# Kernel tuning notes

Measured on AMD Instinct MI355X. Metric: run time of the kernel, lower is better.

## Reference

```python
import jax, jax.numpy as jnp
import numpy as np

B = 2048
NU, NF, NA = 20000, 100000, 20000  # users, feeds, authors
D = 150   # SVD embed dim for FM features
DK = 64   # tag/keyword/d2v embed dim


def setup_inputs() -> dict:
    key = jax.random.key(0)
    ks = jax.random.split(key, 24)
    r = lambda k, shape: (jax.random.normal(k, shape, dtype=jnp.float32) * 0.05)
    # ids: user, feed, author columns with their own vocab ranges
    u = jax.random.randint(ks[0], (B,), 0, NU)
    f = jax.random.randint(ks[1], (B,), 0, NF)
    a = jax.random.randint(ks[2], (B,), 0, NA)
    inputs = jnp.stack([u, f, a], axis=1).astype(jnp.int32)  # [B,3]
    first_order_shifts = jnp.array([0, NU, NU + NF], dtype=jnp.int32)
    return {
        'inputs': inputs,
        'first_order_shifts': first_order_shifts,
        'W_user_feed': r(ks[3], (NU, D)),
        'W_feed_user': r(ks[4], (NF, D)),
        'W_user_author': r(ks[5], (NU, D)),
        'W_author_user': r(ks[6], (NA, D)),
        'W_feed_emb': r(ks[7], (NF, D)),          # trainable=False in original
        'W_user_tag': r(ks[8], (NU, DK)),
        'W_user_key1': r(ks[9], (NU, DK)),
        'W_user_key2': r(ks[10], (NU, DK)),
        'W_feed_tag': r(ks[11], (NF, DK)),
        'W_feed_key1': r(ks[12], (NF, DK)),
        'W_feed_key2': r(ks[13], (NF, DK)),
        'W_uf_d2v': r(ks[14], (NU, DK)),
        'W_fu_d2v': r(ks[15], (NF, DK)),
        'W_ua_d2v': r(ks[16], (NU, DK)),
        'W_au_d2v': r(ks[17], (NA, DK)),
        'W256': r(ks[18], (2 * D * D, 256)),       # 45000 -> 256
        'b256': jnp.zeros((256,), jnp.float32),
        'W128': r(ks[19], (2 * DK * DK, 128)),     # 8192 -> 128
        'b128': jnp.zeros((128,), jnp.float32),
    }


def reference(inputs, first_order_shifts, W_user_feed, W_feed_user,
              W_user_author, W_author_user, W_feed_emb, W_user_tag,
              W_user_key1, W_user_key2, W_feed_tag, W_feed_key1, W_feed_key2,
              W_uf_d2v, W_fu_d2v, W_ua_d2v, W_au_d2v, W256, b256, W128, b128):
    inputs = inputs.reshape(-1, 3)
    u, f, a = inputs[:, 0], inputs[:, 1], inputs[:, 2]
    one_hot_inputs = inputs + first_order_shifts[None, :]

    user_feed_embed = W_user_feed[u]      # [B,150]
    user_author_embed = W_user_author[u]
    author_user_embed = W_author_user[a]
    feed_emb_embed = W_feed_emb[f]
    feed_user_embed = W_feed_user[f]
    user_tag_embed = W_user_tag[u]        # [B,64]
    user_key1_embed = W_user_key1[u]
    user_key2_embed = W_user_key2[u]
    feed_tag_embed = W_feed_tag[f]
    feed_key1_embed = W_feed_key1[f]
    feed_key2_embed = W_feed_key2[f]
    user_feed_d2vem = W_uf_d2v[u]
    user_author_d2vem = W_ua_d2v[u]
    feed_user_d2vem = W_fu_d2v[f]
    author_user_d2vem = W_au_d2v[a]

    # d2v outer products -> [B,64,64] each; concat axis=1 -> [B,128,64]
    user_w_feed = jnp.einsum('bi,bj->bij', user_feed_d2vem, feed_user_d2vem)
    user_w_auth = jnp.einsum('bi,bj->bij', user_author_d2vem, author_user_d2vem)
    user_w_user = jnp.concatenate([user_w_feed, user_w_auth], axis=1)
    user_w_user = user_w_user.reshape(-1, 2 * DK * DK)
    user_w_user = jax.nn.relu(user_w_user @ W128 + b128)  # Dropout inactive (inference)

    # SVD outer products -> [B,150,150] each; concat axis=1 -> [B,300,150]
    user_x_feed = jnp.einsum('bi,bj->bij', user_feed_embed, feed_user_embed)
    user_x_auth = jnp.einsum('bi,bj->bij', user_author_embed, author_user_embed)
    user_x_user = jnp.concatenate([user_x_feed, user_x_auth], axis=1)
    user_x_user = user_x_user.reshape(-1, 2 * D * D)
    user_x_user = jax.nn.relu(user_x_user @ W256 + b256)

    # tf.concat([list], axis=1) stacks the inner list -> [4,B,150], then reshape (-1,4,150)
    embeds_fm = jnp.stack([user_feed_embed, user_author_embed,
                           feed_user_embed, author_user_embed], axis=0)
    fm_embed_inputs = embeds_fm.reshape(-1, 4, D)

    expert_inputs = jnp.concatenate([
        user_feed_embed, user_author_embed, user_tag_embed, user_key1_embed,
        user_key2_embed, user_feed_d2vem, user_author_d2vem, feed_user_embed,
        feed_tag_embed, feed_key1_embed, feed_emb_embed, feed_key2_embed,
        feed_user_d2vem, author_user_embed, author_user_d2vem,
        user_x_user, user_w_user], axis=-1)  # [B,1710]
    return expert_inputs, one_hot_inputs, fm_embed_inputs
```

## Files before the change

### kernel.cpp

```cpp
#include <hip/hip_runtime.h>
#include <hip/hip_bf16.h>
#include <stdint.h>

#define BB   2048
#define DD   150
#define DKK  64

static constexpr int EXPERT_W  = 1774;
static constexpr int X_OFF     = 1390;
static constexpr int W_OFF     = 1646;
static constexpr int EXPERT_SZ = BB * EXPERT_W;
static constexpr int OH_BASE   = EXPERT_SZ;
static constexpr int FM_BASE   = OH_BASE + BB * 3;

static constexpr size_t WTX_OFF = 0;
static constexpr size_t WTW_OFF = 24576000;
static constexpr size_t WSX_OFF = 26673152;
static constexpr size_t WSW_OFF = 60227584;
static constexpr size_t WS_NEED = 77004800;

typedef __attribute__((ext_vector_type(8))) short bf16x8;
typedef __attribute__((ext_vector_type(4))) float f32x4;

union APack { int d[4]; bf16x8 v; };

__device__ __forceinline__ int cvtpk_bf16(float a, float b) {
  int r; asm("v_cvt_pk_bf16_f32 %0, %1, %2" : "=v"(r) : "v"(a), "v"(b)); return r;
}
__device__ __forceinline__ f32x4 mfma16(bf16x8 a, bf16x8 b, f32x4 c) {
  return __builtin_amdgcn_mfma_f32_16x16x32_bf16(a, b, c, 0, 0, 0);
}
__device__ __forceinline__ void gload16(const void* g, void* l) {
  __builtin_amdgcn_global_load_lds(
      (__attribute__((address_space(1))) void*)(g),
      (__attribute__((address_space(3))) void*)(l), 16, 0, 0);
}

__global__ __launch_bounds__(256) void gather_kernel(
    const int* __restrict__ inputs, const int* __restrict__ shifts,
    const float* __restrict__ Wuf, const float* __restrict__ Wfu,
    const float* __restrict__ Wua, const float* __restrict__ Wau,
    const float* __restrict__ Wfe,
    const float* __restrict__ Wut, const float* __restrict__ Wuk1, const float* __restrict__ Wuk2,
    const float* __restrict__ Wft, const float* __restrict__ Wfk1, const float* __restrict__ Wfk2,
    const float* __restrict__ Wufd, const float* __restrict__ Wfud,
    const float* __restrict__ Wuad, const float* __restrict__ Waud,
    float* __restrict__ out)
{
    const int b = blockIdx.x;
    const int u = inputs[b*3 + 0];
    const int f = inputs[b*3 + 1];
    const int a = inputs[b*3 + 2];
    float* row = out + b * EXPERT_W;
    float* fm  = out + FM_BASE;
    const int t = threadIdx.x;

    for (int c = t; c < DD; c += 256) {
        float ufe = Wuf[u*DD + c];
        float uae = Wua[u*DD + c];
        float fue = Wfu[f*DD + c];
        float fee = Wfe[f*DD + c];
        float aue = Wau[a*DD + c];
        row[0    + c] = ufe;
        row[150  + c] = uae;
        row[620  + c] = fue;
        row[898  + c] = fee;
        row[1176 + c] = aue;
        fm[0*BB*DD + b*DD + c] = ufe;
        fm[1*BB*DD + b*DD + c] = uae;
        fm[2*BB*DD + b*DD + c] = fue;
        fm[3*BB*DD + b*DD + c] = aue;
    }
    for (int c = t; c < DKK; c += 256) {
        row[300  + c] = Wut [u*DKK + c];
        row[364  + c] = Wuk1[u*DKK + c];
        row[428  + c] = Wuk2[u*DKK + c];
        row[492  + c] = Wufd[u*DKK + c];
        row[556  + c] = Wuad[u*DKK + c];
        row[770  + c] = Wft [f*DKK + c];
        row[834  + c] = Wfk1[f*DKK + c];
        row[1048 + c] = Wfk2[f*DKK + c];
        row[1112 + c] = Wfud[f*DKK + c];
        row[1326 + c] = Waud[a*DKK + c];
    }
    if (t < 3) {
        out[OH_BASE + b*3 + t] = (float)(inputs[b*3 + t] + shifts[t]);
    }
}

__global__ __launch_bounds__(256) void tile_pack_x(
    const float* __restrict__ W, __hip_bfloat16* __restrict__ Wt)
{
  const int T  = blockIdx.x;
  const int jj = T / 300;
  const int i  = T - jj*300;
  const int t  = threadIdx.x;
  float v[32];
  const float* src = W + ((size_t)i*150 + jj*32)*256 + t;
  #pragma unroll
  for (int jl = 0; jl < 32; ++jl) {
    int j = jj*32 + jl;
    v[jl] = (j < 150) ? src[(size_t)jl*256] : 0.f;
  }
  const int blk = t >> 4, nloc = t & 15;
  char* dst = (char*)Wt + (size_t)T*16384 + (size_t)(blk*512 + nloc*8)*2;
  #pragma unroll
  for (int ksub = 0; ksub < 4; ++ksub) {
    int pk0 = cvtpk_bf16(v[ksub*8+0], v[ksub*8+1]);
    int pk1 = cvtpk_bf16(v[ksub*8+2], v[ksub*8+3]);
    int pk2 = cvtpk_bf16(v[ksub*8+4], v[ksub*8+5]);
    int pk3 = cvtpk_bf16(v[ksub*8+6], v[ksub*8+7]);
    *(int4*)(dst + (size_t)ksub*256) = make_int4(pk0, pk1, pk2, pk3);
  }
}

__global__ __launch_bounds__(128) void tile_pack_w(
    const float* __restrict__ W, __hip_bfloat16* __restrict__ Wt)
{
  const int T  = blockIdx.x;
  const int jj = T >> 7;
  const int i  = T & 127;
  const int t  = threadIdx.x;
  float v[32];
  const float* src = W + ((size_t)i*64 + jj*32)*128 + t;
  #pragma unroll
  for (int jl = 0; jl < 32; ++jl) v[jl] = src[(size_t)jl*128];
  const int blk = t >> 4, nloc = t & 15;
  char* dst = (char*)Wt + (size_t)T*8192 + (size_t)(blk*512 + nloc*8)*2;
  #pragma unroll
  for (int ksub = 0; ksub < 4; ++ksub) {
    int pk0 = cvtpk_bf16(v[ksub*8+0], v[ksub*8+1]);
    int pk1 = cvtpk_bf16(v[ksub*8+2], v[ksub*8+3]);
    int pk2 = cvtpk_bf16(v[ksub*8+4], v[ksub*8+5]);
    int pk3 = cvtpk_bf16(v[ksub*8+6], v[ksub*8+7]);
    *(int4*)(dst + (size_t)ksub*256) = make_int4(pk0, pk1, pk2, pk3);
  }
}

__global__ __launch_bounds__(512, 4) void xuser_mfma(
    const int* __restrict__ inputs,
    const float* __restrict__ Wuf, const float* __restrict__ Wua,
    const float* __restrict__ Wfu, const float* __restrict__ Wau,
    const __hip_bfloat16* __restrict__ WtXt, float* __restrict__ wsX)
{
  __shared__ float xlds[128*20];
  __shared__ __align__(16) __hip_bfloat16 blds[2][8192];

  const int bid = blockIdx.x;
  const int h  = bid & 1;
  const int s  = (bid >> 1) & 15;
  const int mb = bid >> 5;
  const int b0 = mb * 128;
  const bool upper = s >= 8;
  const int sl  = upper ? s - 8 : s;
  const int i0l = sl * 19;
  const int cnt = (150 - i0l) < 19 ? (150 - i0l) : 19;
  const int ig0 = i0l + (upper ? 150 : 0);
  const int tid = threadIdx.x;

  const float* X = upper ? Wua : Wuf;
  const float* Y = upper ? Wau : Wfu;
  const int yoff = upper ? 2 : 1;

  for (int k = tid; k < 128*20; k += 512) {
    int r = k / 20, ii = k - r*20;
    float v = 0.f;
    if (ii < cnt) v = X[(size_t)inputs[(b0+r)*3]*150 + i0l + ii];
    xlds[k] = v;
  }

  const int lane = tid & 63;
  const int w  = tid >> 6;
  const int mg = w >> 1;
  const int ng = w & 1;
  const int lr = lane & 15;
  const int g  = lane >> 4;

  int yid[2];
  #pragma unroll
  for (int mf = 0; mf < 2; ++mf)
    yid[mf] = inputs[(size_t)(b0 + mg*32 + mf*16 + lr)*3 + yoff];

  const char* wtb = (const char*)WtXt + (size_t)h*8192;
  const unsigned wdst = (unsigned)(tid & ~63) * 16;

  auto stageT = [&](int bufi, int T) {
    const char* sp = wtb + (size_t)T*16384 + (size_t)tid*16;
    char* dp = (char*)&blds[bufi][0] + wdst;
    gload16(sp,         dp);
    gload16(sp + 16384, dp + 8192);
  };

  f32x4 acc[2][4];
  #pragma unroll
  for (int i = 0; i < 2; ++i)
    #pragma unroll
    for (int j = 0; j < 4; ++j) acc[i][j] = (f32x4){0.f,0.f,0.f,0.f};

  const int PJ = (cnt + 1) >> 1;
  const int P  = 5 * PJ;

  stageT(0, ig0);
  stageT(1, ig0 + 2);

  int jjc = 0, iic = 0;
  int jjs = 0, iis = 4;
  int yjj = -1;
  float yreg[2][8];

  for (int p = 0; p < P; ++p) {
    if (jjc != yjj) {
      yjj = jjc;
      const int jb = jjc*32 + g*8;
      #pragma unroll
      for (int mf = 0; mf < 2; ++mf) {
        const float* yp = Y + (size_t)yid[mf]*150;
        if (jb + 8 <= 150) {
          #pragma unroll
          for (int hh = 0; hh < 4; ++hh) {
            float2 vv = *(const float2*)(yp + jb + 2*hh);
            yreg[mf][2*hh]   = vv.x;
            yreg[mf][2*hh+1] = vv.y;
          }
        } else {
          #pragma unroll
          for (int e = 0; e < 8; ++e)
            yreg[mf][e] = (jb + e < 150) ? yp[jb + e] : 0.f;
        }
      }
    }
    if (p + 1 < P) asm volatile("s_waitcnt vmcnt(2)" ::: "memory");
    else           asm volatile("s_waitcnt vmcnt(0)" ::: "memory");
    __builtin_amdgcn_s_barrier();
    __builtin_amdgcn_sched_barrier(0);

    const int buf = p & 1;
    const int rem = cnt - iic;
    #pragma unroll
    for (int sc = 0; sc < 2; ++sc) {
      if (sc == 1 && rem < 2) break;
      const __hip_bfloat16* bb = &blds[buf][sc*4096];
      bf16x8 bv[4];
      #pragma unroll
      for (int nf = 0; nf < 4; ++nf)
        bv[nf] = *(const bf16x8*)(bb + (ng*4 + nf)*512 + g*128 + lr*8);
      APack a[2];
      #pragma unroll
      for (int mf = 0; mf < 2; ++mf) {
        float xv = xlds[(mg*32 + mf*16 + lr)*20 + iic + sc];
        #pragma unroll
        for (int e = 0; e < 4; ++e)
          a[mf].d[e] = cvtpk_bf16(xv*yreg[mf][2*e], xv*yreg[mf][2*e+1]);
      }
      #pragma unroll
      for (int mf = 0; mf < 2; ++mf)
        #pragma unroll
        for (int nf = 0; nf < 4; ++nf)
          acc[mf][nf] = mfma16(a[mf].v, bv[nf], acc[mf][nf]);
    }

    __builtin_amdgcn_s_barrier();
    if (p + 2 < P) stageT(buf, jjs*300 + ig0 + iis);

    iic += 2; if (iic >= cnt) { iic = 0; ++jjc; }
    iis += 2; if (iis >= cnt) { iis = 0; ++jjs; }
  }

  float* wp = wsX + ((size_t)s*2048 + b0)*256;
  #pragma unroll
  for (int mf = 0; mf < 2; ++mf) {
    #pragma unroll
    for (int nf = 0; nf < 4; ++nf) {
      int rb  = mg*32 + mf*16 + g*4;
      int col = h*128 + ng*64 + nf*16 + lr;
      f32x4 v = acc[mf][nf];
      #pragma unroll
      for (int e = 0; e < 4; ++e) wp[(size_t)(rb+e)*256 + col] = v[e];
    }
  }
}

__global__ __launch_bounds__(512, 4) void wuser_mfma(
    const int* __restrict__ inputs,
    const float* __restrict__ Wufd, const float* __restrict__ Wuad,
    const float* __restrict__ Wfud, const float* __restrict__ Waud,
    const __hip_bfloat16* __restrict__ WtWt, float* __restrict__ wsW)
{
  __shared__ float xlds[128*8];
  __shared__ __align__(16) __hip_bfloat16 blds[2][8192];

  const int mb = blockIdx.x >> 4;
  const int s  = blockIdx.x & 15;
  const int b0 = mb * 128;
  const bool upper = s >= 8;
  const int i0l = (s & 7) * 8;
  const int ig0 = i0l + (upper ? 64 : 0);
  const int tid = threadIdx.x;

  const float* X = upper ? Wuad : Wufd;
  const float* Y = upper ? Waud : Wfud;
  const int yoff = upper ? 2 : 1;

  for (int k = tid; k < 128*8; k += 512) {
    int r = k >> 3, ii = k & 7;
    xlds[k] = X[(size_t)inputs[(size_t)(b0+r)*3]*64 + i0l + ii];
  }

  const int lane = tid & 63;
  const int w  = tid >> 6;
  const int mg = w >> 1;
  const int ng = w & 1;
  const int lr = lane & 15;
  const int g  = lane >> 4;

  int yid[2];
  #pragma unroll
  for (int mf = 0; mf < 2; ++mf)
    yid[mf] = inputs[(size_t)(b0 + mg*32 + mf*16 + lr)*3 + yoff];

  const char* wtb = (const char*)WtWt;
  const unsigned wdst = (unsigned)(tid & ~63) * 16;

  auto stageT = [&](int bufi, int T) {
    const char* sp = wtb + (size_t)T*8192 + (size_t)tid*16;
    char* dp = (char*)&blds[bufi][0] + wdst;
    gload16(sp,        dp);
    gload16(sp + 8192, dp + 8192);
  };

  f32x4 acc[2][4];
  #pragma unroll
  for (int i = 0; i < 2; ++i)
    #pragma unroll
    for (int j = 0; j < 4; ++j) acc[i][j] = (f32x4){0.f,0.f,0.f,0.f};

  stageT(0, ig0);
  stageT(1, ig0 + 2);

  int jjc = 0, iic = 0;
  int jjs = 0, iis = 4;
  int yjj = -1;
  float yreg[2][8];

  for (int p = 0; p < 8; ++p) {
    if (jjc != yjj) {
      yjj = jjc;
      const int jb = jjc*32 + g*8;
      #pragma unroll
      for (int mf = 0; mf < 2; ++mf) {
        const float* yp = Y + (size_t)yid[mf]*64 + jb;
        #pragma unroll
        for (int hh = 0; hh < 2; ++hh) {
          float4 v = *(const float4*)(yp + hh*4);
          yreg[mf][hh*4]   = v.x;
          yreg[mf][hh*4+1] = v.y;
          yreg[mf][hh*4+2] = v.z;
          yreg[mf][hh*4+3] = v.w;
        }
      }
    }
    if (p + 1 < 8) asm volatile("s_waitcnt vmcnt(2)" ::: "memory");
    else           asm volatile("s_waitcnt vmcnt(0)" ::: "memory");
    __builtin_amdgcn_s_barrier();
    __builtin_amdgcn_sched_barrier(0);

    const int buf = p & 1;
    #pragma unroll
    for (int sc = 0; sc < 2; ++sc) {
      const __hip_bfloat16* bb = &blds[buf][sc*4096];
      bf16x8 bv[4];
      #pragma unroll
      for (int nf = 0; nf < 4; ++nf)
        bv[nf] = *(const bf16x8*)(bb + (ng*4 + nf)*512 + g*128 + lr*8);
      APack a[2];
      #pragma unroll
      for (int mf = 0; mf < 2; ++mf) {
        float xv = xlds[(mg*32 + mf*16 + lr)*8 + iic + sc];
        #pragma unroll
        for (int e = 0; e < 4; ++e)
          a[mf].d[e] = cvtpk_bf16(xv*yreg[mf][2*e], xv*yreg[mf][2*e+1]);
      }
      #pragma unroll
      for (int mf = 0; mf < 2; ++mf)
        #pragma unroll
        for (int nf = 0; nf < 4; ++nf)
          acc[mf][nf] = mfma16(a[mf].v, bv[nf], acc[mf][nf]);
    }

    __builtin_amdgcn_s_barrier();
    if (p + 2 < 8) stageT(buf, jjs*128 + ig0 + iis);

    iic += 2; if (iic >= 8) { iic = 0; ++jjc; }
    iis += 2; if (iis >= 8) { iis = 0; ++jjs; }
  }

  float* wp = wsW + ((size_t)s*2048 + b0)*128;
  #pragma unroll
  for (int mf = 0; mf < 2; ++mf) {
    #pragma unroll
    for (int nf = 0; nf < 4; ++nf) {
      int rb  = mg*32 + mf*16 + g*4;
      int col = ng*64 + nf*16 + lr;
      f32x4 v = acc[mf][nf];
      #pragma unroll
      for (int e = 0; e < 4; ++e) wp[(size_t)(rb+e)*128 + col] = v[e];
    }
  }
}

__global__ __launch_bounds__(256) void epilogue_kernel(
    const float* __restrict__ wsX, const float* __restrict__ wsW,
    const float* __restrict__ b256, const float* __restrict__ b128,
    float* __restrict__ out)
{
  int idx = blockIdx.x*256 + threadIdx.x;
  if (idx >= BB*384) return;
  int b = idx / 384, c = idx - b*384;
  if (c < 256) {
    float acc = b256[c];
    #pragma unroll
    for (int k = 0; k < 16; ++k) acc += wsX[((size_t)k*BB + b)*256 + c];
    out[(size_t)b*EXPERT_W + X_OFF + c] = acc > 0.f ? acc : 0.f;
  } else {
    int cc = c - 256;
    float acc = b128[cc];
    #pragma unroll
    for (int k = 0; k < 16; ++k) acc += wsW[((size_t)k*BB + b)*128 + cc];
    out[(size_t)b*EXPERT_W + W_OFF + cc] = acc > 0.f ? acc : 0.f;
  }
}

static constexpr int NPAIR_X = 300 * 150;
static constexpr int CHX     = 128;

__global__ __launch_bounds__(256) void xuser_kernel(
    const int* __restrict__ inputs,
    const float* __restrict__ Wuf, const float* __restrict__ Wua,
    const float* __restrict__ Wfu, const float* __restrict__ Wau,
    const float* __restrict__ W256, const float* __restrict__ b256,
    float* __restrict__ out)
{
    __shared__ float xs[16][308];
    __shared__ float ys[16][308];
    __shared__ float xy[CHX][16];
    const int half = blockIdx.x & 1;
    const int bg   = blockIdx.x >> 1;
    const int b0   = bg * 16;
    const int t    = threadIdx.x;
    const int bl   = t & 15;
    const int kg   = t >> 4;
    const int kbase = half * 128 + kg * 8;
    for (int idx = t; idx < 16 * DD; idx += 256) {
        int bb = idx / DD;
        int c  = idx - bb * DD;
        int u = inputs[(b0+bb)*3 + 0];
        int f = inputs[(b0+bb)*3 + 1];
        int a = inputs[(b0+bb)*3 + 2];
        xs[bb][c]       = Wuf[u*DD + c];
        xs[bb][150 + c] = Wua[u*DD + c];
        ys[bb][c]       = Wfu[f*DD + c];
        ys[bb][150 + c] = Wau[a*DD + c];
    }
    float acc[8] = {0,0,0,0,0,0,0,0};
    for (int base = 0; base < NPAIR_X; base += CHX) {
        __syncthreads();
        #pragma unroll
        for (int r = 0; r < (CHX*16)/256; ++r) {
            int idx = t + r * 256;
            int pl  = idx >> 4;
            int bb  = idx & 15;
            int p   = base + pl;
            if (p < NPAIR_X) {
                int i = p / 150;
                int j = p - i * 150;
                xy[pl][bb] = xs[bb][i] * ys[bb][(i >= 150 ? 150 : 0) + j];
            }
        }
        __syncthreads();
        const int lim = min(CHX, NPAIR_X - base);
        const float* wp = W256 + base * 256 + kbase;
        for (int pl = 0; pl < lim; ++pl) {
            float sv = xy[pl][bl];
            const float4* w4 = (const float4*)(wp + pl * 256);
            float4 w0 = w4[0], w1 = w4[1];
            acc[0] = fmaf(sv, w0.x, acc[0]); acc[1] = fmaf(sv, w0.y, acc[1]);
            acc[2] = fmaf(sv, w0.z, acc[2]); acc[3] = fmaf(sv, w0.w, acc[3]);
            acc[4] = fmaf(sv, w1.x, acc[4]); acc[5] = fmaf(sv, w1.y, acc[5]);
            acc[6] = fmaf(sv, w1.z, acc[6]); acc[7] = fmaf(sv, w1.w, acc[7]);
        }
    }
    const int rowbase = (b0 + bl) * EXPERT_W + X_OFF;
    #pragma unroll
    for (int m = 0; m < 8; ++m) {
        float v = acc[m] + b256[kbase + m];
        out[rowbase + kbase + m] = (v > 0.f ? v : 0.f);
    }
}

static constexpr int NPAIR_W = 128 * 64;
static constexpr int CHW     = 256;

__global__ __launch_bounds__(256) void wuser_kernel(
    const int* __restrict__ inputs,
    const float* __restrict__ Wufd, const float* __restrict__ Wuad,
    const float* __restrict__ Wfud, const float* __restrict__ Waud,
    const float* __restrict__ W128, const float* __restrict__ b128,
    float* __restrict__ out)
{
    __shared__ float xs[8][132];
    __shared__ float ys[8][132];
    __shared__ float xy[CHW][8];
    const int bg = blockIdx.x;
    const int b0 = bg * 8;
    const int t  = threadIdx.x;
    const int bl = t & 7;
    const int kg = t >> 3;
    const int kbase = kg * 4;
    for (int idx = t; idx < 8 * DKK; idx += 256) {
        int bb = idx >> 6;
        int c  = idx & 63;
        int u = inputs[(b0+bb)*3 + 0];
        int f = inputs[(b0+bb)*3 + 1];
        int a = inputs[(b0+bb)*3 + 2];
        xs[bb][c]      = Wufd[u*DKK + c];
        xs[bb][64 + c] = Wuad[u*DKK + c];
        ys[bb][c]      = Wfud[f*DKK + c];
        ys[bb][64 + c] = Waud[a*DKK + c];
    }
    float acc[4] = {0,0,0,0};
    for (int base = 0; base < NPAIR_W; base += CHW) {
        __syncthreads();
        #pragma unroll
        for (int r = 0; r < (CHW*8)/256; ++r) {
            int idx = t + r * 256;
            int pl  = idx >> 3;
            int bb  = idx & 7;
            int p   = base + pl;
            int i = p >> 6;
            int j = p & 63;
            xy[pl][bb] = xs[bb][i] * ys[bb][(i >= 64 ? 64 : 0) + j];
        }
        __syncthreads();
        const float* wp = W128 + base * 128 + kbase;
        for (int pl = 0; pl < CHW; ++pl) {
            float sv = xy[pl][bl];
            float4 wv = *(const float4*)(wp + pl * 128);
            acc[0] = fmaf(sv, wv.x, acc[0]); acc[1] = fmaf(sv, wv.y, acc[1]);
            acc[2] = fmaf(sv, wv.z, acc[2]); acc[3] = fmaf(sv, wv.w, acc[3]);
        }
    }
    const int rowbase = (b0 + bl) * EXPERT_W + W_OFF;
    #pragma unroll
    for (int m = 0; m < 4; ++m) {
        float v = acc[m] + b128[kbase + m];
        out[rowbase + kbase + m] = (v > 0.f ? v : 0.f);
    }
}

extern "C" void kernel_launch(void* const* d_in, const int* in_sizes, int n_in,
                              void* d_out, int out_size, void* d_ws, size_t ws_size,
                              hipStream_t stream)
{
    const int*   inputs = (const int*)  d_in[0];
    const int*   shifts = (const int*)  d_in[1];
    const float* Wuf    = (const float*)d_in[2];
    const float* Wfu    = (const float*)d_in[3];
    const float* Wua    = (const float*)d_in[4];
    const float* Wau    = (const float*)d_in[5];
    const float* Wfe    = (const float*)d_in[6];
    const float* Wut    = (const float*)d_in[7];
    const float* Wuk1   = (const float*)d_in[8];
    const float* Wuk2   = (const float*)d_in[9];
    const float* Wft    = (const float*)d_in[10];
    const float* Wfk1   = (const float*)d_in[11];
    const float* Wfk2   = (const float*)d_in[12];
    const float* Wufd   = (const float*)d_in[13];
    const float* Wfud   = (const float*)d_in[14];
    const float* Wuad   = (const float*)d_in[15];
    const float* Waud   = (const float*)d_in[16];
    const float* W256   = (const float*)d_in[17];
    const float* b256   = (const float*)d_in[18];
    const float* W128   = (const float*)d_in[19];
    const float* b128   = (const float*)d_in[20];

    float* out = (float*)d_out;

    gather_kernel<<<BB, 256, 0, stream>>>(inputs, shifts,
        Wuf, Wfu, Wua, Wau, Wfe, Wut, Wuk1, Wuk2, Wft, Wfk1, Wfk2,
        Wufd, Wfud, Wuad, Waud, out);

    if (ws_size >= WS_NEED) {
        char* ws = (char*)d_ws;
        __hip_bfloat16* WtX = (__hip_bfloat16*)(ws + WTX_OFF);
        __hip_bfloat16* WtW = (__hip_bfloat16*)(ws + WTW_OFF);
        float* wsX = (float*)(ws + WSX_OFF);
        float* wsW = (float*)(ws + WSW_OFF);

        tile_pack_x<<<1500, 256, 0, stream>>>(W256, WtX);
        tile_pack_w<<<256, 128, 0, stream>>>(W128, WtW);

        xuser_mfma<<<512, 512, 0, stream>>>(inputs, Wuf, Wua, Wfu, Wau, WtX, wsX);
        wuser_mfma<<<256, 512, 0, stream>>>(inputs, Wufd, Wuad, Wfud, Waud, WtW, wsW);

        epilogue_kernel<<<(BB*384 + 255)/256, 256, 0, stream>>>(wsX, wsW, b256, b128, out);
    } else {
        xuser_kernel<<<256, 256, 0, stream>>>(inputs, Wuf, Wua, Wfu, Wau, W256, b256, out);
        wuser_kernel<<<256, 256, 0, stream>>>(inputs, Wufd, Wuad, Wfud, Waud, W128, b128, out);
    }
}
```

Baseline: 105.7 us.

## Switch X-path GEMM to 32x32x16 MFMA with 2x4 wave tiling

Replaces the 16x16x32 bf16 MFMA tiles in the user-x-user projection kernel with 32x32x16 MFMAs. Waves are remapped from a 4x2 to a 2x4 grid, and the outer-product A-operand construction and output scatter are reworked for the larger tile. This reduces the number of MFMA issues and B-fragment LDS reads per step. The double-buffer prefetch is also changed from a two-deep vmcnt-based pipeline to a one-ahead stage with __syncthreads, which may expose more global-load latency.

Measured after the change: 121.6 us. +15.0%, slower.

```diff
diff --git a/kernel.cpp b/kernel.cpp
--- a/kernel.cpp
+++ b/kernel.cpp
@@ -19,8 +19,9 @@
 static constexpr size_t WSW_OFF = 60227584;
 static constexpr size_t WS_NEED = 77004800;
 
-typedef __attribute__((ext_vector_type(8))) short bf16x8;
-typedef __attribute__((ext_vector_type(4))) float f32x4;
+typedef __attribute__((ext_vector_type(8)))  short bf16x8;
+typedef __attribute__((ext_vector_type(4)))  float f32x4;
+typedef __attribute__((ext_vector_type(16))) float f32x16;
 
 union APack { int d[4]; bf16x8 v; };
 
@@ -29,6 +30,9 @@
 }
 __device__ __forceinline__ f32x4 mfma16(bf16x8 a, bf16x8 b, f32x4 c) {
   return __builtin_amdgcn_mfma_f32_16x16x32_bf16(a, b, c, 0, 0, 0);
+}
+__device__ __forceinline__ f32x16 mfma32(bf16x8 a, bf16x8 b, f32x16 c) {
+  return __builtin_amdgcn_mfma_f32_32x32x16_bf16(a, b, c, 0, 0, 0);
 }
 __device__ __forceinline__ void gload16(const void* g, void* l) {
   __builtin_amdgcn_global_load_lds(
@@ -170,19 +174,24 @@
   }
 
   const int lane = tid & 63;
-  const int w  = tid >> 6;
-  const int mg = w >> 1;
-  const int ng = w & 1;
-  const int lr = lane & 15;
-  const int g  = lane >> 4;
+  const int w    = tid >> 6;
+  const int mg   = w >> 2;
+  const int ng   = w & 3;
+  const int lr32 = lane & 31;
+  const int hi   = lane >> 5;
+  const int lr16 = lane & 15;
+  const int q    = lr32 >> 4;
 
   int yid[2];
   #pragma unroll
   for (int mf = 0; mf < 2; ++mf)
-    yid[mf] = inputs[(size_t)(b0 + mg*32 + mf*16 + lr)*3 + yoff];
+    yid[mf] = inputs[(size_t)(b0 + mg*64 + mf*32 + lr32)*3 + yoff];
 
   const char* wtb = (const char*)WtXt + (size_t)h*8192;
   const unsigned wdst = (unsigned)(tid & ~63) * 16;
+
+  const int boff0 = (ng*2 + q)*512 + hi*128 + lr16*8;
+  const int boff1 = boff0 + 256;
 
   auto stageT = [&](int bufi, int T) {
     const char* sp = wtb + (size_t)T*16384 + (size_t)tid*16;
@@ -191,91 +200,88 @@
     gload16(sp + 16384, dp + 8192);
   };
 
-  f32x4 acc[2][4];
-  #pragma unroll
-  for (int i = 0; i < 2; ++i)
-    #pragma unroll
-    for (int j = 0; j < 4; ++j) acc[i][j] = (f32x4){0.f,0.f,0.f,0.f};
+  f32x16 acc[2];
+  #pragma unroll
+  for (int mf = 0; mf < 2; ++mf)
+    #pragma unroll
+    for (int e = 0; e < 16; ++e) acc[mf][e] = 0.f;
 
   const int PJ = (cnt + 1) >> 1;
   const int P  = 5 * PJ;
 
   stageT(0, ig0);
-  stageT(1, ig0 + 2);
+  __syncthreads();
 
   int jjc = 0, iic = 0;
-  int jjs = 0, iis = 4;
   int yjj = -1;
-  float yreg[2][8];
+  float yreg[2][16];
+  int buf = 0;
 
   for (int p = 0; p < P; ++p) {
+    {
+      int njj = jjc, nii = iic + 2;
+      if (nii >= cnt) { njj++; nii = 0; }
+      if (njj < 5) stageT(buf^1, njj*300 + ig0 + nii);
+    }
     if (jjc != yjj) {
       yjj = jjc;
-      const int jb = jjc*32 + g*8;
       #pragma unroll
       for (int mf = 0; mf < 2; ++mf) {
         const float* yp = Y + (size_t)yid[mf]*150;
-        if (jb + 8 <= 150) {
-          #pragma unroll
-          for (int hh = 0; hh < 4; ++hh) {
-            float2 vv = *(const float2*)(yp + jb + 2*hh);
-            yreg[mf][2*hh]   = vv.x;
-            yreg[mf][2*hh+1] = vv.y;
+        #pragma unroll
+        for (int r8 = 0; r8 < 2; ++r8) {
+          const int s0 = jjc*32 + r8*16 + hi*8;
+          if (s0 + 8 <= 150) {
+            #pragma unroll
+            for (int hh = 0; hh < 4; ++hh) {
+              float2 vv = *(const float2*)(yp + s0 + 2*hh);
+              yreg[mf][r8*8 + 2*hh]   = vv.x;
+              yreg[mf][r8*8 + 2*hh+1] = vv.y;
+            }
+          } else {
+            #pragma unroll
+            for (int e = 0; e < 8; ++e)
+              yreg[mf][r8*8 + e] = (s0 + e < 150) ? yp[s0 + e] : 0.f;
           }
-        } else {
-          #pragma unroll
-          for (int e = 0; e < 8; ++e)
-            yreg[mf][e] = (jb + e < 150) ? yp[jb + e] : 0.f;
         }
       }
     }
-    if (p + 1 < P) asm volatile("s_waitcnt vmcnt(2)" ::: "memory");
-    else           asm volatile("s_waitcnt vmcnt(0)" ::: "memory");
-    __builtin_amdgcn_s_barrier();
-    __builtin_amdgcn_sched_barrier(0);
-
-    const int buf = p & 1;
+
     const int rem = cnt - iic;
     #pragma unroll
     for (int sc = 0; sc < 2; ++sc) {
       if (sc == 1 && rem < 2) break;
       const __hip_bfloat16* bb = &blds[buf][sc*4096];
-      bf16x8 bv[4];
+      const float xv0 = xlds[(mg*64 +  0 + lr32)*20 + iic + sc];
+      const float xv1 = xlds[(mg*64 + 32 + lr32)*20 + iic + sc];
       #pragma unroll
-      for (int nf = 0; nf < 4; ++nf)
-        bv[nf] = *(const bf16x8*)(bb + (ng*4 + nf)*512 + g*128 + lr*8);
-      APack a[2];
-      #pragma unroll
-      for (int mf = 0; mf < 2; ++mf) {
-        float xv = xlds[(mg*32 + mf*16 + lr)*20 + iic + sc];
+      for (int kstep = 0; kstep < 2; ++kstep) {
+        bf16x8 bv = *(const bf16x8*)(bb + (kstep ? boff1 : boff0));
+        APack a0, a1;
         #pragma unroll
-        for (int e = 0; e < 4; ++e)
-          a[mf].d[e] = cvtpk_bf16(xv*yreg[mf][2*e], xv*yreg[mf][2*e+1]);
+        for (int e2 = 0; e2 < 4; ++e2) {
+          a0.d[e2] = cvtpk_bf16(xv0*yreg[0][kstep*8 + 2*e2], xv0*yreg[0][kstep*8 + 2*e2 + 1]);
+          a1.d[e2] = cvtpk_bf16(xv1*yreg[1][kstep*8 + 2*e2], xv1*yreg[1][kstep*8 + 2*e2 + 1]);
+        }
+        acc[0] = mfma32(a0.v, bv, acc[0]);
+        acc[1] = mfma32(a1.v, bv, acc[1]);
       }
-      #pragma unroll
-      for (int mf = 0; mf < 2; ++mf)
-        #pragma unroll
-        for (int nf = 0; nf < 4; ++nf)
-          acc[mf][nf] = mfma16(a[mf].v, bv[nf], acc[mf][nf]);
-    }
-
-    __builtin_amdgcn_s_barrier();
-    if (p + 2 < P) stageT(buf, jjs*300 + ig0 + iis);
-
+    }
+
+    __syncthreads();
+    buf ^= 1;
     iic += 2; if (iic >= cnt) { iic = 0; ++jjc; }
-    iis += 2; if (iis >= cnt) { iis = 0; ++jjs; }
   }
 
   float* wp = wsX + ((size_t)s*2048 + b0)*256;
+  const int col = h*128 + ng*32 + lr32;
   #pragma unroll
   for (int mf = 0; mf < 2; ++mf) {
     #pragma unroll
-    for (int nf = 0; nf < 4; ++nf) {
-      int rb  = mg*32 + mf*16 + g*4;
-      int col = h*128 + ng*64 + nf*16 + lr;
-      f32x4 v = acc[mf][nf];
-      #pragma unroll
-      for (int e = 0; e < 4; ++e) wp[(size_t)(rb+e)*256 + col] = v[e];
+    for (int e = 0; e < 16; ++e) {
+      const int rowf = (e & 3) + 8*(e >> 2) + 4*hi;
+      const int rb = mg*64 + mf*32 + rowf;
+      wp[(size_t)rb*256 + col] = acc[mf][e];
     }
   }
 }
```

## Stage three K-steps per pipeline window and store split-K partials in bf16

Applied to the files above, without the earlier changes.

The xuser MFMA kernel now loads three K-tiles per LDS window instead of two, so there are fewer barrier and wait cycles per unit of work. It also drops the wasted half-steps that occurred when cnt was odd, and raises wave priority during the MFMA section. The split-K partial sums written by both MFMA kernels and read by the epilogue are now bf16 instead of fp32, which halves workspace traffic. In exchange, each partial is rounded to bf16 before the 16-way reduction, which costs accuracy. The larger LDS buffer may also lower occupancy.

Result: faster. 99.09 us (-6.3%).

```diff
diff --git a/kernel.cpp b/kernel.cpp
--- a/kernel.cpp
+++ b/kernel.cpp
@@ -16,8 +16,8 @@
 static constexpr size_t WTX_OFF = 0;
 static constexpr size_t WTW_OFF = 24576000;
 static constexpr size_t WSX_OFF = 26673152;
-static constexpr size_t WSW_OFF = 60227584;
-static constexpr size_t WS_NEED = 77004800;
+static constexpr size_t WSW_OFF = 43450368;
+static constexpr size_t WS_NEED = 51838976;
 
 typedef __attribute__((ext_vector_type(8))) short bf16x8;
 typedef __attribute__((ext_vector_type(4))) float f32x4;
@@ -141,10 +141,10 @@
     const int* __restrict__ inputs,
     const float* __restrict__ Wuf, const float* __restrict__ Wua,
     const float* __restrict__ Wfu, const float* __restrict__ Wau,
-    const __hip_bfloat16* __restrict__ WtXt, float* __restrict__ wsX)
+    const __hip_bfloat16* __restrict__ WtXt, __hip_bfloat16* __restrict__ wsX)
 {
   __shared__ float xlds[128*20];
-  __shared__ __align__(16) __hip_bfloat16 blds[2][8192];
+  __shared__ __align__(16) __hip_bfloat16 blds[2][3*4096];
 
   const int bid = blockIdx.x;
   const int h  = bid & 1;
@@ -184,11 +184,15 @@
   const char* wtb = (const char*)WtXt + (size_t)h*8192;
   const unsigned wdst = (unsigned)(tid & ~63) * 16;
 
-  auto stageT = [&](int bufi, int T) {
-    const char* sp = wtb + (size_t)T*16384 + (size_t)tid*16;
-    char* dp = (char*)&blds[bufi][0] + wdst;
-    gload16(sp,         dp);
-    gload16(sp + 16384, dp + 8192);
+  int jjs = 0, iis = 0;
+  auto stageWin = [&](int bufi) {
+    #pragma unroll
+    for (int q = 0; q < 3; ++q) {
+      const char* sp = wtb + (size_t)(jjs*300 + ig0 + iis)*16384 + (size_t)tid*16;
+      gload16(sp, (char*)&blds[bufi][0] + (unsigned)q*8192 + wdst);
+      if (iis + 1 < cnt) ++iis;
+      else if (jjs + 1 < 5) { iis = 0; ++jjs; }
+    }
   };
 
   f32x4 acc[2][4];
@@ -197,49 +201,49 @@
     #pragma unroll
     for (int j = 0; j < 4; ++j) acc[i][j] = (f32x4){0.f,0.f,0.f,0.f};
 
-  const int PJ = (cnt + 1) >> 1;
-  const int P  = 5 * PJ;
-
-  stageT(0, ig0);
-  stageT(1, ig0 + 2);
+  const int P = 5 * cnt;
+  const int W = (P + 2) / 3;
+
+  stageWin(0);
+  stageWin(1);
 
   int jjc = 0, iic = 0;
-  int jjs = 0, iis = 4;
   int yjj = -1;
   float yreg[2][8];
 
-  for (int p = 0; p < P; ++p) {
-    if (jjc != yjj) {
-      yjj = jjc;
-      const int jb = jjc*32 + g*8;
-      #pragma unroll
-      for (int mf = 0; mf < 2; ++mf) {
-        const float* yp = Y + (size_t)yid[mf]*150;
-        if (jb + 8 <= 150) {
-          #pragma unroll
-          for (int hh = 0; hh < 4; ++hh) {
-            float2 vv = *(const float2*)(yp + jb + 2*hh);
-            yreg[mf][2*hh]   = vv.x;
-            yreg[mf][2*hh+1] = vv.y;
+  for (int wi = 0; wi < W; ++wi) {
+    if (wi + 1 < W) asm volatile("s_waitcnt vmcnt(3)" ::: "memory");
+    else            asm volatile("s_waitcnt vmcnt(0)" ::: "memory");
+    __builtin_amdgcn_s_barrier();
+    __builtin_amdgcn_sched_barrier(0);
+    __builtin_amdgcn_s_setprio(1);
+
+    const int buf = wi & 1;
+    const int base = wi * 3;
+    #pragma unroll
+    for (int q = 0; q < 3; ++q) {
+      if (base + q >= P) break;
+      if (jjc != yjj) {
+        yjj = jjc;
+        const int jb = jjc*32 + g*8;
+        #pragma unroll
+        for (int mf = 0; mf < 2; ++mf) {
+          const float* yp = Y + (size_t)yid[mf]*150;
+          if (jb + 8 <= 150) {
+            #pragma unroll
+            for (int hh = 0; hh < 4; ++hh) {
+              float2 vv = *(const float2*)(yp + jb + 2*hh);
+              yreg[mf][2*hh]   = vv.x;
+              yreg[mf][2*hh+1] = vv.y;
+            }
+          } else {
+            #pragma unroll
+            for (int e = 0; e < 8; ++e)
+              yreg[mf][e] = (jb + e < 150) ? yp[jb + e] : 0.f;
           }
-        } else {
-          #pragma unroll
-          for (int e = 0; e < 8; ++e)
-            yreg[mf][e] = (jb + e < 150) ? yp[jb + e] : 0.f;
         }
       }
-    }
-    if (p + 1 < P) asm volatile("s_waitcnt vmcnt(2)" ::: "memory");
-    else           asm volatile("s_waitcnt vmcnt(0)" ::: "memory");
-    __builtin_amdgcn_s_barrier();
-    __builtin_amdgcn_sched_barrier(0);
-
-    const int buf = p & 1;
-    const int rem = cnt - iic;
-    #pragma unroll
-    for (int sc = 0; sc < 2; ++sc) {
-      if (sc == 1 && rem < 2) break;
-      const __hip_bfloat16* bb = &blds[buf][sc*4096];
+      const __hip_bfloat16* bb = &blds[buf][q*4096];
       bf16x8 bv[4];
       #pragma unroll
       for (int nf = 0; nf < 4; ++nf)
@@ -247,7 +251,7 @@
       APack a[2];
       #pragma unroll
       for (int mf = 0; mf < 2; ++mf) {
-        float xv = xlds[(mg*32 + mf*16 + lr)*20 + iic + sc];
+        const float xv = xlds[(mg*32 + mf*16 + lr)*20 + iic];
         #pragma unroll
         for (int e = 0; e < 4; ++e)
           a[mf].d[e] = cvtpk_bf16(xv*yreg[mf][2*e], xv*yreg[mf][2*e+1]);
@@ -257,16 +261,15 @@
         #pragma unroll
         for (int nf = 0; nf < 4; ++nf)
           acc[mf][nf] = mfma16(a[mf].v, bv[nf], acc[mf][nf]);
-    }
-
+      ++iic; if (iic >= cnt) { iic = 0; ++jjc; }
+    }
+
+    __builtin_amdgcn_s_setprio(0);
     __builtin_amdgcn_s_barrier();
-    if (p + 2 < P) stageT(buf, jjs*300 + ig0 + iis);
-
-    iic += 2; if (iic >= cnt) { iic = 0; ++jjc; }
-    iis += 2; if (iis >= cnt) { iis = 0; ++jjs; }
-  }
-
-  float* wp = wsX + ((size_t)s*2048 + b0)*256;
+    if (wi + 2 < W) stageWin(buf);
+  }
+
+  __hip_bfloat16* wp = wsX + ((size_t)s*2048 + b0)*256;
   #pragma unroll
   for (int mf = 0; mf < 2; ++mf) {
     #pragma unroll
@@ -275,7 +278,8 @@
       int col = h*128 + ng*64 + nf*16 + lr;
       f32x4 v = acc[mf][nf];
       #pragma unroll
-      for (int e = 0; e < 4; ++e) wp[(size_t)(rb+e)*256 + col] = v[e];
+      for (int e = 0; e < 4; ++e)
+        wp[(size_t)(rb+e)*256 + col] = __float2bfloat16(v[e]);
     }
   }
 }
@@ -284,7 +288,7 @@
     const int* __restrict__ inputs,
     const float* __restrict__ Wufd, const float* __restrict__ Wuad,
     const float* __restrict__ Wfud, const float* __restrict__ Waud,
-    const __hip_bfloat16* __restrict__ WtWt, float* __restrict__ wsW)
+    const __hip_bfloat16* __restrict__ WtWt, __hip_bfloat16* __restrict__ wsW)
 {
   __shared__ float xlds[128*8];
   __shared__ __align__(16) __hip_bfloat16 blds[2][8192];
@@ -394,7 +398,7 @@
     iis += 2; if (iis >= 8) { iis = 0; ++jjs; }
   }
 
-  float* wp = wsW + ((size_t)s*2048 + b0)*128;
+  __hip_bfloat16* wp = wsW + ((size_t)s*2048 + b0)*128;
   #pragma unroll
   for (int mf = 0; mf < 2; ++mf) {
     #pragma unroll
@@ -403,13 +407,14 @@
       int col = ng*64 + nf*16 + lr;
       f32x4 v = acc[mf][nf];
       #pragma unroll
-      for (int e = 0; e < 4; ++e) wp[(size_t)(rb+e)*128 + col] = v[e];
+      for (int e = 0; e < 4; ++e)
+        wp[(size_t)(rb+e)*128 + col] = __float2bfloat16(v[e]);
     }
   }
 }
 
 __global__ __launch_bounds__(256) void epilogue_kernel(
-    const float* __restrict__ wsX, const float* __restrict__ wsW,
+    const __hip_bfloat16* __restrict__ wsX, const __hip_bfloat16* __restrict__ wsW,
     const float* __restrict__ b256, const float* __restrict__ b128,
     float* __restrict__ out)
 {
@@ -419,13 +424,15 @@
   if (c < 256) {
     float acc = b256[c];
     #pragma unroll
-    for (int k = 0; k < 16; ++k) acc += wsX[((size_t)k*BB + b)*256 + c];
+    for (int k = 0; k < 16; ++k)
+      acc += __bfloat162float(wsX[((size_t)k*BB + b)*256 + c]);
     out[(size_t)b*EXPERT_W + X_OFF + c] = acc > 0.f ? acc : 0.f;
   } else {
     int cc = c - 256;
     float acc = b128[cc];
     #pragma unroll
-    for (int k = 0; k < 16; ++k) acc += wsW[((size_t)k*BB + b)*128 + cc];
+    for (int k = 0; k < 16; ++k)
+      acc += __bfloat162float(wsW[((size_t)k*BB + b)*128 + cc]);
     out[(size_t)b*EXPERT_W + W_OFF + cc] = acc > 0.f ? acc : 0.f;
   }
 }
@@ -593,8 +600,8 @@
         char* ws = (char*)d_ws;
         __hip_bfloat16* WtX = (__hip_bfloat16*)(ws + WTX_OFF);
         __hip_bfloat16* WtW = (__hip_bfloat16*)(ws + WTW_OFF);
-        float* wsX = (float*)(ws + WSX_OFF);
-        float* wsW = (float*)(ws + WSW_OFF);
+        __hip_bfloat16* wsX = (__hip_bfloat16*)(ws + WSX_OFF);
+        __hip_bfloat16* wsW = (__hip_bfloat16*)(ws + WSW_OFF);
 
         tile_pack_x<<<1500, 256, 0, stream>>>(W256, WtX);
         tile_pack_w<<<256, 128, 0, stream>>>(W128, WtW);
```
